# Kernel optimization log

Hardware: AMD Instinct MI355X
Metric: run time of the kernel (lower is better)

## Reference

```python
import jax, jax.numpy as jnp
import numpy as np

B, S, D = 8, 2048, 64
NEG = -1e9


def setup_inputs() -> dict:
    key = jax.random.key(0)
    kq, kk, kv = jax.random.split(key, 3)
    return {
        "queries": jax.random.normal(kq, (B, S, D), dtype=jnp.float32),
        "keys": jax.random.normal(kk, (B, S, D), dtype=jnp.float32),
        "values": jax.random.normal(kv, (B, S, D), dtype=jnp.float32),
        "mask_q": jnp.ones((B, S), dtype=jnp.float32),
        "mask_k": jnp.ones((B, S), dtype=jnp.float32),
        "mask_v": jnp.ones((B, S), dtype=jnp.float32),
    }


def reference(queries, keys, values, mask_q, mask_k, mask_v):
    # scaled QK^T: [B, Sq, Sk]
    scaler = jnp.sqrt(jnp.asarray(queries.shape[-1], dtype=queries.dtype))
    scores = jnp.einsum("bqd,bkd->bqk", queries, keys) / scaler
    # additive padding mask from outer product of query/key masks
    padding_mask = mask_q[:, :, None] * mask_k[:, None, :]  # [B, Sq, Sk]
    scores = scores + (1.0 - padding_mask) * NEG
    attention_weights = jax.nn.softmax(scores, axis=-1)
    # mask values then weighted sum
    values = values * mask_v[:, :, None]
    output = jnp.einsum("bqk,bkd->bqd", attention_weights, values)
    return output
```

## Files before the change

kernel.cpp:

```cpp
#include <hip/hip_runtime.h>
#include <hip/hip_bf16.h>
#include <math.h>

#define BATCH 8
#define SEQ   2048
#define DIM   64
#define NEGC  (-1e9f)

typedef short short8  __attribute__((ext_vector_type(8)));
typedef float f32x4   __attribute__((ext_vector_type(4)));
typedef float f32x16  __attribute__((ext_vector_type(16)));

#define MFMA32(a, b, c) __builtin_amdgcn_mfma_f32_32x32x16_bf16((a), (b), (c), 0, 0, 0)

__device__ __forceinline__ ushort f2bf(float x) {
    uint u = __float_as_uint(x);
    uint r = (u + 0x7fffu + ((u >> 16) & 1u)) >> 16;
    return (ushort)r;
}
__device__ __forceinline__ float bf2f(ushort h) {
    return __uint_as_float(((uint)h) << 16);
}

__global__ __launch_bounds__(256)
void prep_kv(const float* __restrict__ K, const float* __restrict__ V,
             const float* __restrict__ MV, ushort* __restrict__ ws) {
    __shared__ float raw[64 * 68];
    const int t    = threadIdx.x;
    const int b    = blockIdx.x >> 5;
    const int tile = blockIdx.x & 31;
    const float* Kb  = K  + ((size_t)b * SEQ + tile * 64) * DIM;
    const float* Vb  = V  + ((size_t)b * SEQ + tile * 64) * DIM;
    const float* MVb = MV + (size_t)b * SEQ + tile * 64;
    ushort* wsI = ws + (size_t)(b * 32 + tile) * 8192;

#pragma unroll
    for (int u = 0; u < 4; u++) {
        int f = t + 256 * u, key = f >> 4, d4 = (f & 15) * 4;
        *(float4*)&raw[key * 68 + d4] = *(const float4*)(Kb + (size_t)f * 4);
    }
    __syncthreads();
#pragma unroll
    for (int u = 0; u < 2; u++) {
        int r = t + 256 * u;
        int mt = r >> 8, kc = (r >> 6) & 3, L = r & 63;
        int key = mt * 32 + (L & 31), d0 = kc * 16 + (L >> 5) * 8;
        float4 x0 = *(float4*)&raw[key * 68 + d0];
        float4 x1 = *(float4*)&raw[key * 68 + d0 + 4];
        float xs[8] = {x0.x, x0.y, x0.z, x0.w, x1.x, x1.y, x1.z, x1.w};
        short8 hv;
#pragma unroll
        for (int j = 0; j < 8; j++) hv[j] = (short)f2bf(xs[j]);
        *(short8*)(wsI + r * 8) = hv;
    }
    __syncthreads();

#pragma unroll
    for (int u = 0; u < 4; u++) {
        int f = t + 256 * u, key = f >> 4, d4 = (f & 15) * 4;
        float4 x = *(const float4*)(Vb + (size_t)f * 4);
        float mv = MVb[key];
        x.x *= mv; x.y *= mv; x.z *= mv; x.w *= mv;
        *(float4*)&raw[key * 68 + d4] = x;
    }
    __syncthreads();
#pragma unroll
    for (int u = 0; u < 2; u++) {
        int r = t + 256 * u;
        int dt = r >> 8, kc = (r >> 6) & 3, L = r & 63;
        int d = dt * 32 + (L & 31), k0 = kc * 16 + (L >> 5) * 8;
        short8 ov;
#pragma unroll
        for (int j = 0; j < 8; j++) ov[j] = (short)f2bf(raw[(k0 + j) * 68 + d]);
        *(short8*)(wsI + 4096 + r * 8) = ov;
    }
}

__global__ __launch_bounds__(256, 2)
void attn_main(const float* __restrict__ Q, const float* __restrict__ MQ,
               const float* __restrict__ MK, const ushort* __restrict__ ws,
               float* __restrict__ PO, float* __restrict__ ML) {
    __shared__ __align__(16) ushort Stage[2][8192];
    __shared__ __align__(16) float  Msc[2][64 * 34];

    const int t    = threadIdx.x;
    const int w    = t >> 6;
    const int lane = t & 63;
    const int h    = lane >> 5;
    const int lm   = lane & 31;
    const int qg   = w & 1;
    const int kh   = w >> 1;

    const int s  = blockIdx.x & 1;
    const int qb = blockIdx.x >> 1;
    const int b  = qb >> 5;
    const int qt = qb & 31;
    const int q  = qt * 64 + qg * 32 + lm;

    const float*  MKb  = MK + (size_t)b * SEQ;
    const ushort* wsKV = ws + (size_t)b * 32 * 8192;

    short8 qh[4], ql[4];
    {
        const float* Qr = Q + ((size_t)b * SEQ + q) * DIM;
#pragma unroll
        for (int kc = 0; kc < 4; kc++) {
            const float* p = Qr + kc * 16 + h * 8;
            float4 x0 = *(const float4*)p;
            float4 x1 = *(const float4*)(p + 4);
            float xs[8] = {x0.x, x0.y, x0.z, x0.w, x1.x, x1.y, x1.z, x1.w};
#pragma unroll
            for (int j = 0; j < 8; j++) {
                float v   = xs[j] * 0.125f;
                ushort hi = f2bf(v);
                ql[kc][j] = (short)f2bf(v - bf2f(hi));
                qh[kc][j] = (short)hi;
            }
        }
    }
    const float mq   = MQ[(size_t)b * SEQ + q];
    const float apen = NEGC * mq;

    float m = -1e30f, l = 0.0f;
    f32x16 ot0, ot1;
#pragma unroll
    for (int i = 0; i < 16; i++) { ot0[i] = 0.0f; ot1[i] = 0.0f; }

    {
        const ushort* src = wsKV + (size_t)(s * 16) * 8192;
#pragma unroll
        for (int u = 0; u < 4; u++) {
            const int off = (u * 256 + w * 64 + lane) * 8;
            __builtin_amdgcn_global_load_lds(
                (const __attribute__((address_space(1))) void*)(src + off),
                (__attribute__((address_space(3))) void*)(&Stage[0][0] + off),
                16, 0, 0);
        }
    }
    __syncthreads();

    f32x4 mk[4];
#pragma unroll
    for (int v = 0; v < 4; v++)
        mk[v] = *(const f32x4*)(MKb + (s * 16) * 64 + kh * 32 + v * 8 + h * 4);

#pragma unroll 1
    for (int tt = 0; tt < 16; tt++) {
        const ushort* cur = &Stage[tt & 1][0];

        if (tt + 1 < 16) {
            const ushort* src = wsKV + (size_t)(s * 16 + tt + 1) * 8192;
            ushort* dst = &Stage[(tt + 1) & 1][0];
#pragma unroll
            for (int u = 0; u < 4; u++) {
                const int off = (u * 256 + w * 64 + lane) * 8;
                __builtin_amdgcn_global_load_lds(
                    (const __attribute__((address_space(1))) void*)(src + off),
                    (__attribute__((address_space(3))) void*)(dst + off),
                    16, 0, 0);
            }
        }
        f32x4 nmk[4];
#pragma unroll
        for (int v = 0; v < 4; v++) nmk[v] = mk[v];
        if (tt + 1 < 16) {
            const float* mkp = MKb + (s * 16 + tt + 1) * 64 + kh * 32 + h * 4;
#pragma unroll
            for (int v = 0; v < 4; v++) nmk[v] = *(const f32x4*)(mkp + v * 8);
        }

        f32x16 st;
#pragma unroll
        for (int i = 0; i < 16; i++) st[i] = 0.0f;
#pragma unroll
        for (int kc = 0; kc < 4; kc++) {
            short8 a = *(const short8*)&cur[((kh * 4 + kc) * 64 + lane) * 8];
            st = MFMA32(a, qh[kc], st);
            st = MFMA32(a, ql[kc], st);
        }

        float sv[16];
#pragma unroll
        for (int v = 0; v < 4; v++)
#pragma unroll
            for (int c = 0; c < 4; c++)
                sv[v * 4 + c] = st[v * 4 + c] + (NEGC - apen * mk[v][c]);
        float cm = sv[0];
#pragma unroll
        for (int i = 1; i < 16; i++) cm = fmaxf(cm, sv[i]);
        cm = fmaxf(cm, __shfl_xor(cm, 32));
        float nm    = fmaxf(m, cm);
        float alpha = __expf(m - nm);
        m = nm;

        float p[16], cs = 0.0f;
#pragma unroll
        for (int i = 0; i < 16; i++) { p[i] = __expf(sv[i] - nm); cs += p[i]; }
        cs += __shfl_xor(cs, 32);
        l   = l * alpha + cs;
        ot0 *= alpha; ot1 *= alpha;

        uint g[4][2], x[4][2];
#pragma unroll
        for (int v = 0; v < 4; v++) {
            __hip_bfloat162 c0 = __float22bfloat162_rn(make_float2(p[v*4+0], p[v*4+1]));
            __hip_bfloat162 c1 = __float22bfloat162_rn(make_float2(p[v*4+2], p[v*4+3]));
            __builtin_memcpy(&g[v][0], &c0, 4);
            __builtin_memcpy(&g[v][1], &c1, 4);
            x[v][0] = (uint)__shfl_xor((int)g[v][0], 32);
            x[v][1] = (uint)__shfl_xor((int)g[v][1], 32);
        }
        uint pbw[2][4];
        pbw[0][0] = h ? x[1][0] : g[0][0];
        pbw[0][1] = h ? x[1][1] : g[0][1];
        pbw[0][2] = h ? g[1][0] : x[0][0];
        pbw[0][3] = h ? g[1][1] : x[0][1];
        pbw[1][0] = h ? x[3][0] : g[2][0];
        pbw[1][1] = h ? x[3][1] : g[2][1];
        pbw[1][2] = h ? g[3][0] : x[2][0];
        pbw[1][3] = h ? g[3][1] : x[2][1];

#pragma unroll
        for (int c = 0; c < 2; c++) {
            short8 pb;
            __builtin_memcpy(&pb, &pbw[c][0], 16);
            short8 v0 = *(const short8*)&cur[4096 + ((0 * 4 + kh * 2 + c) * 64 + lane) * 8];
            short8 v1 = *(const short8*)&cur[4096 + ((1 * 4 + kh * 2 + c) * 64 + lane) * 8];
            ot0 = MFMA32(v0, pb, ot0);
            ot1 = MFMA32(v1, pb, ot1);
        }

#pragma unroll
        for (int v = 0; v < 4; v++) mk[v] = nmk[v];
        __syncthreads();
    }

    if (kh == 1) {
        float* sc = &Msc[qg][lane * 34];
#pragma unroll
        for (int i = 0; i < 16; i++) { sc[i] = ot0[i]; sc[16 + i] = ot1[i]; }
        sc[32] = m;
        sc[33] = l;
    }
    __syncthreads();
    if (kh == 0) {
        const float* sc = &Msc[qg][lane * 34];
        float mb = sc[32], lb = sc[33];
        float nm = fmaxf(m, mb);
        float fa = __expf(m - nm);
        float fb = __expf(mb - nm);
        float lt = l * fa + lb * fb;

        float* po = PO + (((size_t)(s * 8 + b) * 32 + qt) * 64 + qg * 32 + lm) * 64;
#pragma unroll
        for (int dt = 0; dt < 2; dt++) {
            const f32x16& o = dt ? ot1 : ot0;
#pragma unroll
            for (int rq = 0; rq < 4; rq++) {
                f32x4 r;
#pragma unroll
                for (int c = 0; c < 4; c++)
                    r[c] = o[rq * 4 + c] * fa + sc[dt * 16 + rq * 4 + c] * fb;
                *(f32x4*)(po + dt * 32 + rq * 8 + h * 4) = r;
            }
        }
        if (h == 0) {
            float2* ml2 = (float2*)ML;
            ml2[((size_t)(s * 8 + b) * 32 + qt) * 64 + qg * 32 + lm] =
                make_float2(nm, lt);
        }
    }
}

__global__ __launch_bounds__(256)
void merge_o(const float* __restrict__ PO, const float* __restrict__ ML,
             float* __restrict__ O) {
    const int tid = blockIdx.x * 256 + threadIdx.x;
    const int qln = tid >> 4;
    const int dq  = tid & 15;
    const int b   = qln >> 11;
    const int qr  = qln & 2047;
    const int qt  = qr >> 6;
    const int qq  = qr & 63;

    const float2* ml2 = (const float2*)ML;
    const size_t mlidx = ((size_t)b * 32 + qt) * 64 + qq;
    float2 A = ml2[mlidx];
    float2 Bv = ml2[(size_t)8 * 32 * 64 + mlidx];
    float mm = fmaxf(A.x, Bv.x);
    float fa = __expf(A.x - mm);
    float fb = __expf(Bv.x - mm);
    float inv = 1.0f / (A.y * fa + Bv.y * fb);

    const size_t o0 = (((size_t)b * 32 + qt) * 64 + qq) * 64 + dq * 4;
    f32x4 va = *(const f32x4*)(PO + o0);
    f32x4 vb = *(const f32x4*)(PO + (size_t)8 * 32 * 64 * 64 + o0);
    f32x4 r = (va * fa + vb * fb) * inv;
    *(f32x4*)(O + ((size_t)b * SEQ + qr) * DIM + dq * 4) = r;
}

extern "C" void kernel_launch(void* const* d_in, const int* in_sizes, int n_in,
                              void* d_out, int out_size, void* d_ws, size_t ws_size,
                              hipStream_t stream) {
    const float* Q  = (const float*)d_in[0];
    const float* K  = (const float*)d_in[1];
    const float* V  = (const float*)d_in[2];
    const float* MQ = (const float*)d_in[3];
    const float* MK = (const float*)d_in[4];
    const float* MV = (const float*)d_in[5];
    float* O = (float*)d_out;

    ushort* wsKV = (ushort*)d_ws;
    float*  PO   = (float*)((char*)d_ws + (4u << 20));
    float*  ML   = (float*)((char*)d_ws + (12u << 20));

    prep_kv  <<<dim3(256),  dim3(256), 0, stream>>>(K, V, MV, wsKV);
    attn_main<<<dim3(512),  dim3(256), 0, stream>>>(Q, MQ, MK, wsKV, PO, ML);
    merge_o  <<<dim3(1024), dim3(256), 0, stream>>>(PO, ML, O);
}
```

Measured before the change: 101.7 us.

## Split key range four ways across blocks and merge partials

Raises the split-K factor from 2 to 4, so the attention kernel launches 1024 blocks that each process 8 key tiles instead of 16. The merge kernel now combines four partial outputs using log-sum-exp rescaling. The separate merge scratch is aliased into the staging LDS and launch bounds are raised to allow 4 blocks per CU, both aimed at more concurrent waves on the 256 CUs. The cost is twice the partial-output traffic, a heavier merge pass, and shorter loops with more prologue overhead per block.

```diff
diff --git a/kernel.cpp b/kernel.cpp
--- a/kernel.cpp
+++ b/kernel.cpp
@@ -6,6 +6,8 @@
 #define SEQ   2048
 #define DIM   64
 #define NEGC  (-1e9f)
+#define SPLIT 4
+#define TPB   8
 
 typedef short short8  __attribute__((ext_vector_type(8)));
 typedef float f32x4   __attribute__((ext_vector_type(4)));
@@ -76,12 +78,11 @@
     }
 }
 
-__global__ __launch_bounds__(256, 2)
+__global__ __launch_bounds__(256, 4)
 void attn_main(const float* __restrict__ Q, const float* __restrict__ MQ,
                const float* __restrict__ MK, const ushort* __restrict__ ws,
                float* __restrict__ PO, float* __restrict__ ML) {
     __shared__ __align__(16) ushort Stage[2][8192];
-    __shared__ __align__(16) float  Msc[2][64 * 34];
 
     const int t    = threadIdx.x;
     const int w    = t >> 6;
@@ -91,8 +92,8 @@
     const int qg   = w & 1;
     const int kh   = w >> 1;
 
-    const int s  = blockIdx.x & 1;
-    const int qb = blockIdx.x >> 1;
+    const int s  = blockIdx.x & 3;
+    const int qb = blockIdx.x >> 2;
     const int b  = qb >> 5;
     const int qt = qb & 31;
     const int q  = qt * 64 + qg * 32 + lm;
@@ -127,7 +128,7 @@
     for (int i = 0; i < 16; i++) { ot0[i] = 0.0f; ot1[i] = 0.0f; }
 
     {
-        const ushort* src = wsKV + (size_t)(s * 16) * 8192;
+        const ushort* src = wsKV + (size_t)(s * TPB) * 8192;
 #pragma unroll
         for (int u = 0; u < 4; u++) {
             const int off = (u * 256 + w * 64 + lane) * 8;
@@ -142,14 +143,14 @@
     f32x4 mk[4];
 #pragma unroll
     for (int v = 0; v < 4; v++)
-        mk[v] = *(const f32x4*)(MKb + (s * 16) * 64 + kh * 32 + v * 8 + h * 4);
+        mk[v] = *(const f32x4*)(MKb + (s * TPB) * 64 + kh * 32 + v * 8 + h * 4);
 
 #pragma unroll 1
-    for (int tt = 0; tt < 16; tt++) {
+    for (int tt = 0; tt < TPB; tt++) {
         const ushort* cur = &Stage[tt & 1][0];
 
-        if (tt + 1 < 16) {
-            const ushort* src = wsKV + (size_t)(s * 16 + tt + 1) * 8192;
+        if (tt + 1 < TPB) {
+            const ushort* src = wsKV + (size_t)(s * TPB + tt + 1) * 8192;
             ushort* dst = &Stage[(tt + 1) & 1][0];
 #pragma unroll
             for (int u = 0; u < 4; u++) {
@@ -163,8 +164,8 @@
         f32x4 nmk[4];
 #pragma unroll
         for (int v = 0; v < 4; v++) nmk[v] = mk[v];
-        if (tt + 1 < 16) {
-            const float* mkp = MKb + (s * 16 + tt + 1) * 64 + kh * 32 + h * 4;
+        if (tt + 1 < TPB) {
+            const float* mkp = MKb + (s * TPB + tt + 1) * 64 + kh * 32 + h * 4;
 #pragma unroll
             for (int v = 0; v < 4; v++) nmk[v] = *(const f32x4*)(mkp + v * 8);
         }
@@ -235,8 +236,9 @@
         __syncthreads();
     }
 
+    float* MscF = (float*)&Stage[0][0];
     if (kh == 1) {
-        float* sc = &Msc[qg][lane * 34];
+        float* sc = MscF + (qg * 64 + lane) * 36;
 #pragma unroll
         for (int i = 0; i < 16; i++) { sc[i] = ot0[i]; sc[16 + i] = ot1[i]; }
         sc[32] = m;
@@ -244,14 +246,14 @@
     }
     __syncthreads();
     if (kh == 0) {
-        const float* sc = &Msc[qg][lane * 34];
+        const float* sc = MscF + (qg * 64 + lane) * 36;
         float mb = sc[32], lb = sc[33];
         float nm = fmaxf(m, mb);
         float fa = __expf(m - nm);
         float fb = __expf(mb - nm);
         float lt = l * fa + lb * fb;
 
-        float* po = PO + (((size_t)(s * 8 + b) * 32 + qt) * 64 + qg * 32 + lm) * 64;
+        float* po = PO + (((size_t)(s * 8 + b) * SEQ) + qt * 64 + qg * 32 + lm) * 64;
 #pragma unroll
         for (int dt = 0; dt < 2; dt++) {
             const f32x16& o = dt ? ot1 : ot0;
@@ -266,7 +268,7 @@
         }
         if (h == 0) {
             float2* ml2 = (float2*)ML;
-            ml2[((size_t)(s * 8 + b) * 32 + qt) * 64 + qg * 32 + lm] =
+            ml2[((size_t)(s * 8 + b) * SEQ) + qt * 64 + qg * 32 + lm] =
                 make_float2(nm, lt);
         }
     }
@@ -280,23 +282,31 @@
     const int dq  = tid & 15;
     const int b   = qln >> 11;
     const int qr  = qln & 2047;
-    const int qt  = qr >> 6;
-    const int qq  = qr & 63;
 
     const float2* ml2 = (const float2*)ML;
-    const size_t mlidx = ((size_t)b * 32 + qt) * 64 + qq;
-    float2 A = ml2[mlidx];
-    float2 Bv = ml2[(size_t)8 * 32 * 64 + mlidx];
-    float mm = fmaxf(A.x, Bv.x);
-    float fa = __expf(A.x - mm);
-    float fb = __expf(Bv.x - mm);
-    float inv = 1.0f / (A.y * fa + Bv.y * fb);
-
-    const size_t o0 = (((size_t)b * 32 + qt) * 64 + qq) * 64 + dq * 4;
-    f32x4 va = *(const f32x4*)(PO + o0);
-    f32x4 vb = *(const f32x4*)(PO + (size_t)8 * 32 * 64 * 64 + o0);
-    f32x4 r = (va * fa + vb * fb) * inv;
-    *(f32x4*)(O + ((size_t)b * SEQ + qr) * DIM + dq * 4) = r;
+    const size_t MLS = (size_t)8 * SEQ;
+    float2 mls[SPLIT];
+#pragma unroll
+    for (int s = 0; s < SPLIT; s++) mls[s] = ml2[(size_t)(s * 8 + b) * SEQ + qr];
+    float mm = mls[0].x;
+#pragma unroll
+    for (int s = 1; s < SPLIT; s++) mm = fmaxf(mm, mls[s].x);
+    float f[SPLIT], denom = 0.0f;
+#pragma unroll
+    for (int s = 0; s < SPLIT; s++) {
+        f[s] = __expf(mls[s].x - mm);
+        denom += mls[s].y * f[s];
+    }
+    float inv = 1.0f / denom;
+
+    const size_t POS = (size_t)8 * SEQ * 64;
+    const size_t o0  = ((size_t)b * SEQ + qr) * 64 + dq * 4;
+    f32x4 acc = {0, 0, 0, 0};
+#pragma unroll
+    for (int s = 0; s < SPLIT; s++)
+        acc += (*(const f32x4*)(PO + s * POS + o0)) * f[s];
+    *(f32x4*)(O + ((size_t)b * SEQ + qr) * DIM + dq * 4) = acc * inv;
+    (void)MLS;
 }
 
 extern "C" void kernel_launch(void* const* d_in, const int* in_sizes, int n_in,
@@ -312,9 +322,9 @@
 
     ushort* wsKV = (ushort*)d_ws;
     float*  PO   = (float*)((char*)d_ws + (4u << 20));
-    float*  ML   = (float*)((char*)d_ws + (12u << 20));
+    float*  ML   = (float*)((char*)d_ws + (20u << 20));
 
     prep_kv  <<<dim3(256),  dim3(256), 0, stream>>>(K, V, MV, wsKV);
-    attn_main<<<dim3(512),  dim3(256), 0, stream>>>(Q, MQ, MK, wsKV, PO, ML);
+    attn_main<<<dim3(1024), dim3(256), 0, stream>>>(Q, MQ, MK, wsKV, PO, ML);
     merge_o  <<<dim3(1024), dim3(256), 0, stream>>>(PO, ML, O);
 }
```

Result: no change. 101.8 us (+0.0%).
